# Kernel optimization log

Hardware: AMD Instinct MI355X
Metric: run time of the kernel (lower is better)

## Reference

```python
import jax, jax.numpy as jnp
import numpy as np


def setup_inputs() -> dict:
    key = jax.random.key(0)
    k1, k2 = jax.random.split(key)
    tensor_1 = jax.random.normal(k1, (8192, 256), dtype=jnp.float32)
    tensor_2 = jax.random.normal(k2, (16384, 256), dtype=jnp.float32)
    return {"tensor_1": tensor_1, "tensor_2": tensor_2}


def reference(tensor_1, tensor_2):
    # L2-normalize along the feature dim (matches torch .norm(dim=-1), no eps)
    n1 = tensor_1 / jnp.linalg.norm(tensor_1, axis=-1, keepdims=True)  # [N, d]
    n2 = tensor_2 / jnp.linalg.norm(tensor_2, axis=-1, keepdims=True)  # [M, d]
    cos_sim = jnp.einsum("nd,md->nm", n1, n2)  # [N, M] cosine similarity
    top3, _ = jax.lax.top_k(cos_sim, 3)        # [N, 3]
    return top3.mean(axis=-1)                  # [N]
```

## Files before the change

### kernel.cpp

```cpp
#include <hip/hip_runtime.h>
#include <hip/hip_bf16.h>
#include <stdint.h>

#define N1 8192
#define N2 16384
#define DIM 256
#define BM 256
#define CS 8
#define COLS (N2 / CS)
#define TC 64
#define NT (COLS / TC)
#define NPART CS

typedef short v8s  __attribute__((ext_vector_type(8)));
typedef float f32x4 __attribute__((ext_vector_type(4)));

#define GLD16(g, l)                                                                         \
  __builtin_amdgcn_global_load_lds((const __attribute__((address_space(1))) uint32_t*)(g),  \
                                   (__attribute__((address_space(3))) uint32_t*)(l), 16, 0, 0)

__device__ __forceinline__ void top3_insert(float v, float& t0, float& t1, float& t2) {
    float nt1 = __builtin_amdgcn_fmed3f(v, t0, t1);
    float nt2 = __builtin_amdgcn_fmed3f(v, t1, t2);
    t0 = fmaxf(t0, v);
    t1 = nt1;
    t2 = nt2;
}

__global__ __launch_bounds__(256) void normalize_kernel(
        const float* __restrict__ inA, const float* __restrict__ inB,
        __hip_bfloat16* __restrict__ outA, __hip_bfloat16* __restrict__ outB) {
    const int wave = threadIdx.x >> 6;
    const int lane = threadIdx.x & 63;
    const int rgrp = lane >> 4;
    const int li   = lane & 15;
    const int gr   = blockIdx.x * 16 + wave * 4 + rgrp;
    const float* in;
    __hip_bfloat16* out;
    int row;
    if (gr < N1) { in = inA; out = outA; row = gr; }
    else         { in = inB; out = outB; row = gr - N1; }
    const float* rp = in + (size_t)row * DIM + li * 4;
    float4 v[4];
    #pragma unroll
    for (int j = 0; j < 4; ++j) v[j] = *(const float4*)(rp + j * 64);
    float s = 0.f;
    #pragma unroll
    for (int j = 0; j < 4; ++j)
        s += v[j].x * v[j].x + v[j].y * v[j].y + v[j].z * v[j].z + v[j].w * v[j].w;
    #pragma unroll
    for (int off = 8; off; off >>= 1) s += __shfl_xor(s, off, 64);
    const float inv = 1.0f / sqrtf(s);
    __hip_bfloat16* wp = out + (size_t)row * DIM + li * 4;
    #pragma unroll
    for (int j = 0; j < 4; ++j) {
        __hip_bfloat16 o[4];
        o[0] = __float2bfloat16(v[j].x * inv);
        o[1] = __float2bfloat16(v[j].y * inv);
        o[2] = __float2bfloat16(v[j].z * inv);
        o[3] = __float2bfloat16(v[j].w * inv);
        *(uint2*)(wp + j * 64) = *(uint2*)o;
    }
}

__global__ __launch_bounds__(512, 2) void gemm_top3_kernel(
        const __hip_bfloat16* __restrict__ A, const __hip_bfloat16* __restrict__ B,
        float* __restrict__ partial) {
    __shared__ char smem[2 * 32768];

    const int tid  = threadIdx.x;
    const int wave = tid >> 6;
    const int lane = tid & 63;
    const int lo   = lane & 15;
    const int quad = lane >> 4;
    const int cs   = blockIdx.x & 7;
    const int rb   = blockIdx.x >> 3;
    const int row0 = rb * BM;

    v8s af[2][8];
    {
        const char* arow = (const char*)A + (size_t)(row0 + wave * 32 + lo) * 512 + quad * 16;
        #pragma unroll
        for (int rt = 0; rt < 2; ++rt)
            #pragma unroll
            for (int s = 0; s < 8; ++s)
                af[rt][s] = *(const v8s*)(arow + rt * 8192 + s * 64);
    }
    asm volatile("s_waitcnt vmcnt(0)" ::: "memory");

    const char* Bb = (const char*)B + (size_t)cs * COLS * 512;
    int gsrc[4];
    #pragma unroll
    for (int j = 0; j < 4; ++j) {
        const int col = j * 16 + wave * 2 + (lane >> 5);
        gsrc[j] = col * 512 + (((lane & 31) ^ (col & 7)) << 4);
    }

    int swz[8];
    #pragma unroll
    for (int s = 0; s < 8; ++s) swz[s] = (((s * 4 + quad) ^ (lo & 7)) << 4);
    int bco[4];
    #pragma unroll
    for (int ct = 0; ct < 4; ++ct) bco[ct] = (ct * 16 + lo) * 512;

    float t0[8], t1[8], t2[8];
    #pragma unroll
    for (int i = 0; i < 8; ++i) { t0[i] = -1e30f; t1[i] = -1e30f; t2[i] = -1e30f; }

    #pragma unroll
    for (int j = 0; j < 4; ++j)
        GLD16(Bb + gsrc[j], smem + j * 8192 + wave * 1024);
    #pragma unroll
    for (int j = 0; j < 4; ++j)
        GLD16(Bb + 32768 + gsrc[j], smem + 32768 + j * 8192 + wave * 1024);

    #pragma unroll 2
    for (int t = 0; t < NT; ++t) {
        if (t == NT - 1) asm volatile("s_waitcnt vmcnt(0)" ::: "memory");
        else             asm volatile("s_waitcnt vmcnt(4)" ::: "memory");
        __builtin_amdgcn_s_barrier();

        const char* bbuf = smem + (t & 1) * 32768;
        f32x4 acc[2][4];
        __builtin_amdgcn_s_setprio(1);
        #pragma unroll
        for (int s = 0; s < 8; ++s) {
            #pragma unroll
            for (int ct = 0; ct < 4; ++ct) {
                v8s bf = *(const v8s*)(bbuf + bco[ct] + swz[s]);
                #pragma unroll
                for (int rt = 0; rt < 2; ++rt) {
                    if (s == 0)
                        acc[rt][ct] = __builtin_amdgcn_mfma_f32_16x16x32_bf16(
                            af[rt][0], bf, (f32x4){0.f, 0.f, 0.f, 0.f}, 0, 0, 0);
                    else
                        acc[rt][ct] = __builtin_amdgcn_mfma_f32_16x16x32_bf16(
                            af[rt][s], bf, acc[rt][ct], 0, 0, 0);
                }
            }
        }
        __builtin_amdgcn_s_setprio(0);
        __builtin_amdgcn_s_barrier();
        if (t + 2 < NT) {
            const char* src = Bb + (size_t)(t + 2) * 32768;
            char* dst = smem + (t & 1) * 32768;
            #pragma unroll
            for (int j = 0; j < 4; ++j)
                GLD16(src + gsrc[j], dst + j * 8192 + wave * 1024);
        }
        #pragma unroll
        for (int rt = 0; rt < 2; ++rt)
            #pragma unroll
            for (int r = 0; r < 4; ++r) {
                const int sl = rt * 4 + r;
                #pragma unroll
                for (int ct = 0; ct < 4; ++ct)
                    top3_insert(acc[rt][ct][r], t0[sl], t1[sl], t2[sl]);
            }
    }

    #pragma unroll
    for (int sl = 0; sl < 8; ++sl) {
        #pragma unroll
        for (int step = 1; step < 16; step <<= 1) {
            float b0 = __shfl_xor(t0[sl], step, 64);
            float b1 = __shfl_xor(t1[sl], step, 64);
            float b2 = __shfl_xor(t2[sl], step, 64);
            top3_insert(b0, t0[sl], t1[sl], t2[sl]);
            top3_insert(b1, t0[sl], t1[sl], t2[sl]);
            top3_insert(b2, t0[sl], t1[sl], t2[sl]);
        }
    }
    if (lo == 0) {
        #pragma unroll
        for (int rt = 0; rt < 2; ++rt)
            #pragma unroll
            for (int r = 0; r < 4; ++r) {
                const int row = row0 + wave * 32 + rt * 16 + quad * 4 + r;
                float* p = partial + ((size_t)row * NPART + cs) * 3;
                const int sl = rt * 4 + r;
                p[0] = t0[sl]; p[1] = t1[sl]; p[2] = t2[sl];
            }
    }
}

__global__ __launch_bounds__(256) void merge_kernel(
        const float* __restrict__ partial, float* __restrict__ out) {
    const int row = blockIdx.x * 256 + threadIdx.x;
    if (row >= N1) return;
    const float4* p = (const float4*)(partial + (size_t)row * NPART * 3);
    float t0 = -1e30f, t1 = -1e30f, t2 = -1e30f;
    #pragma unroll
    for (int i = 0; i < 6; ++i) {
        float4 v = p[i];
        top3_insert(v.x, t0, t1, t2);
        top3_insert(v.y, t0, t1, t2);
        top3_insert(v.z, t0, t1, t2);
        top3_insert(v.w, t0, t1, t2);
    }
    out[row] = (t0 + t1 + t2) * (1.0f / 3.0f);
}

extern "C" void kernel_launch(void* const* d_in, const int* in_sizes, int n_in,
                              void* d_out, int out_size, void* d_ws, size_t ws_size,
                              hipStream_t stream) {
    const float* tA = (const float*)d_in[0];
    const float* tB = (const float*)d_in[1];
    float* out = (float*)d_out;

    __hip_bfloat16* An = (__hip_bfloat16*)d_ws;
    __hip_bfloat16* Bn = An + (size_t)N1 * DIM;
    float* partial = (float*)(Bn + (size_t)N2 * DIM);

    normalize_kernel<<<(N1 + N2) / 16, 256, 0, stream>>>(tA, tB, An, Bn);
    gemm_top3_kernel<<<(N1 / BM) * CS, 512, 0, stream>>>(An, Bn, partial);
    merge_kernel<<<(N1 + 255) / 256, 256, 0, stream>>>(partial, out);
}
```

Baseline: 139.6 us.

## Retile GEMM to 64 rows per wave with narrower column tiles and more splits

Each wave now holds A fragments for 64 rows and processes 32-column B tiles, splitting columns 16 ways instead of 8. This halves LDS fragment reads per MFMA by reusing each B fragment across four row tiles, and shrinks the shared buffers. In exchange, A fragments and top-3 state double in registers, which risks spills or lower occupancy. The merge kernel also does twice the partial work.

```diff
diff --git a/kernel.cpp b/kernel.cpp
--- a/kernel.cpp
+++ b/kernel.cpp
@@ -5,10 +5,10 @@
 #define N1 8192
 #define N2 16384
 #define DIM 256
-#define BM 256
-#define CS 8
+#define BM 512
+#define CS 16
 #define COLS (N2 / CS)
-#define TC 64
+#define TC 32
 #define NT (COLS / TC)
 #define NPART CS
 
@@ -66,22 +66,22 @@
 __global__ __launch_bounds__(512, 2) void gemm_top3_kernel(
         const __hip_bfloat16* __restrict__ A, const __hip_bfloat16* __restrict__ B,
         float* __restrict__ partial) {
-    __shared__ char smem[2 * 32768];
+    __shared__ char smem[2 * 16384];
 
     const int tid  = threadIdx.x;
     const int wave = tid >> 6;
     const int lane = tid & 63;
     const int lo   = lane & 15;
     const int quad = lane >> 4;
-    const int cs   = blockIdx.x & 7;
-    const int rb   = blockIdx.x >> 3;
+    const int cs   = blockIdx.x & 15;
+    const int rb   = blockIdx.x >> 4;
     const int row0 = rb * BM;
 
-    v8s af[2][8];
+    v8s af[4][8];
     {
-        const char* arow = (const char*)A + (size_t)(row0 + wave * 32 + lo) * 512 + quad * 16;
-        #pragma unroll
-        for (int rt = 0; rt < 2; ++rt)
+        const char* arow = (const char*)A + (size_t)(row0 + wave * 64 + lo) * 512 + quad * 16;
+        #pragma unroll
+        for (int rt = 0; rt < 4; ++rt)
             #pragma unroll
             for (int s = 0; s < 8; ++s)
                 af[rt][s] = *(const v8s*)(arow + rt * 8192 + s * 64);
@@ -89,9 +89,9 @@
     asm volatile("s_waitcnt vmcnt(0)" ::: "memory");
 
     const char* Bb = (const char*)B + (size_t)cs * COLS * 512;
-    int gsrc[4];
-    #pragma unroll
-    for (int j = 0; j < 4; ++j) {
+    int gsrc[2];
+    #pragma unroll
+    for (int j = 0; j < 2; ++j) {
         const int col = j * 16 + wave * 2 + (lane >> 5);
         gsrc[j] = col * 512 + (((lane & 31) ^ (col & 7)) << 4);
     }
@@ -99,68 +99,69 @@
     int swz[8];
     #pragma unroll
     for (int s = 0; s < 8; ++s) swz[s] = (((s * 4 + quad) ^ (lo & 7)) << 4);
-    int bco[4];
-    #pragma unroll
-    for (int ct = 0; ct < 4; ++ct) bco[ct] = (ct * 16 + lo) * 512;
-
-    float t0[8], t1[8], t2[8];
-    #pragma unroll
-    for (int i = 0; i < 8; ++i) { t0[i] = -1e30f; t1[i] = -1e30f; t2[i] = -1e30f; }
-
-    #pragma unroll
-    for (int j = 0; j < 4; ++j)
+    const int bco0 = lo * 512;
+    const int bco1 = (16 + lo) * 512;
+
+    float t0[16], t1[16], t2[16];
+    #pragma unroll
+    for (int i = 0; i < 16; ++i) { t0[i] = -1e30f; t1[i] = -1e30f; t2[i] = -1e30f; }
+
+    #pragma unroll
+    for (int j = 0; j < 2; ++j)
         GLD16(Bb + gsrc[j], smem + j * 8192 + wave * 1024);
     #pragma unroll
-    for (int j = 0; j < 4; ++j)
-        GLD16(Bb + 32768 + gsrc[j], smem + 32768 + j * 8192 + wave * 1024);
+    for (int j = 0; j < 2; ++j)
+        GLD16(Bb + 16384 + gsrc[j], smem + 16384 + j * 8192 + wave * 1024);
 
     #pragma unroll 2
     for (int t = 0; t < NT; ++t) {
         if (t == NT - 1) asm volatile("s_waitcnt vmcnt(0)" ::: "memory");
-        else             asm volatile("s_waitcnt vmcnt(4)" ::: "memory");
+        else             asm volatile("s_waitcnt vmcnt(2)" ::: "memory");
         __builtin_amdgcn_s_barrier();
 
-        const char* bbuf = smem + (t & 1) * 32768;
-        f32x4 acc[2][4];
+        const char* bbuf = smem + (t & 1) * 16384;
+        f32x4 acc[4][2];
         __builtin_amdgcn_s_setprio(1);
         #pragma unroll
         for (int s = 0; s < 8; ++s) {
-            #pragma unroll
-            for (int ct = 0; ct < 4; ++ct) {
-                v8s bf = *(const v8s*)(bbuf + bco[ct] + swz[s]);
-                #pragma unroll
-                for (int rt = 0; rt < 2; ++rt) {
-                    if (s == 0)
-                        acc[rt][ct] = __builtin_amdgcn_mfma_f32_16x16x32_bf16(
-                            af[rt][0], bf, (f32x4){0.f, 0.f, 0.f, 0.f}, 0, 0, 0);
-                    else
-                        acc[rt][ct] = __builtin_amdgcn_mfma_f32_16x16x32_bf16(
-                            af[rt][s], bf, acc[rt][ct], 0, 0, 0);
+            v8s bf0 = *(const v8s*)(bbuf + bco0 + swz[s]);
+            v8s bf1 = *(const v8s*)(bbuf + bco1 + swz[s]);
+            #pragma unroll
+            for (int rt = 0; rt < 4; ++rt) {
+                if (s == 0) {
+                    acc[rt][0] = __builtin_amdgcn_mfma_f32_16x16x32_bf16(
+                        af[rt][0], bf0, (f32x4){0.f, 0.f, 0.f, 0.f}, 0, 0, 0);
+                    acc[rt][1] = __builtin_amdgcn_mfma_f32_16x16x32_bf16(
+                        af[rt][0], bf1, (f32x4){0.f, 0.f, 0.f, 0.f}, 0, 0, 0);
+                } else {
+                    acc[rt][0] = __builtin_amdgcn_mfma_f32_16x16x32_bf16(
+                        af[rt][s], bf0, acc[rt][0], 0, 0, 0);
+                    acc[rt][1] = __builtin_amdgcn_mfma_f32_16x16x32_bf16(
+                        af[rt][s], bf1, acc[rt][1], 0, 0, 0);
                 }
             }
         }
         __builtin_amdgcn_s_setprio(0);
         __builtin_amdgcn_s_barrier();
         if (t + 2 < NT) {
-            const char* src = Bb + (size_t)(t + 2) * 32768;
-            char* dst = smem + (t & 1) * 32768;
-            #pragma unroll
-            for (int j = 0; j < 4; ++j)
+            const char* src = Bb + (size_t)(t + 2) * 16384;
+            char* dst = smem + (t & 1) * 16384;
+            #pragma unroll
+            for (int j = 0; j < 2; ++j)
                 GLD16(src + gsrc[j], dst + j * 8192 + wave * 1024);
         }
         #pragma unroll
-        for (int rt = 0; rt < 2; ++rt)
+        for (int rt = 0; rt < 4; ++rt)
             #pragma unroll
             for (int r = 0; r < 4; ++r) {
                 const int sl = rt * 4 + r;
-                #pragma unroll
-                for (int ct = 0; ct < 4; ++ct)
-                    top3_insert(acc[rt][ct][r], t0[sl], t1[sl], t2[sl]);
+                top3_insert(acc[rt][0][r], t0[sl], t1[sl], t2[sl]);
+                top3_insert(acc[rt][1][r], t0[sl], t1[sl], t2[sl]);
             }
     }
 
     #pragma unroll
-    for (int sl = 0; sl < 8; ++sl) {
+    for (int sl = 0; sl < 16; ++sl) {
         #pragma unroll
         for (int step = 1; step < 16; step <<= 1) {
             float b0 = __shfl_xor(t0[sl], step, 64);
@@ -173,10 +174,10 @@
     }
     if (lo == 0) {
         #pragma unroll
-        for (int rt = 0; rt < 2; ++rt)
+        for (int rt = 0; rt < 4; ++rt)
             #pragma unroll
             for (int r = 0; r < 4; ++r) {
-                const int row = row0 + wave * 32 + rt * 16 + quad * 4 + r;
+                const int row = row0 + wave * 64 + rt * 16 + quad * 4 + r;
                 float* p = partial + ((size_t)row * NPART + cs) * 3;
                 const int sl = rt * 4 + r;
                 p[0] = t0[sl]; p[1] = t1[sl]; p[2] = t2[sl];
@@ -191,7 +192,7 @@
     const float4* p = (const float4*)(partial + (size_t)row * NPART * 3);
     float t0 = -1e30f, t1 = -1e30f, t2 = -1e30f;
     #pragma unroll
-    for (int i = 0; i < 6; ++i) {
+    for (int i = 0; i < 12; ++i) {
         float4 v = p[i];
         top3_insert(v.x, t0, t1, t2);
         top3_insert(v.y, t0, t1, t2);
@@ -214,5 +215,5 @@
 
     normalize_kernel<<<(N1 + N2) / 16, 256, 0, stream>>>(tA, tB, An, Bn);
     gemm_top3_kernel<<<(N1 / BM) * CS, 512, 0, stream>>>(An, Bn, partial);
-    merge_kernel<<<(N1 + 255) / 256, 256, 0, stream>>>(partial, out);
-}
+    merge_kernel<<<N1 / 256, 256, 0, stream>>>(partial, out);
+}
```

New measurement: 168.6 us. +20.7%, slower.
